# Kernel tuning notes

Hardware: AMD Instinct MI355X
Metric: run time of the kernel (lower is better)

The kernel has to match this reference:

```python
import jax, jax.numpy as jnp
import numpy as np

N_NODES = 100000
N_EDGES = 1600000
IN_DIM = 128
HID_DIM = 128


def setup_inputs() -> dict:
    key = jax.random.key(0)
    k_x, k_e, k_w1, k_w2 = jax.random.split(key, 4)
    x = jax.random.normal(k_x, (N_NODES, IN_DIM), dtype=jnp.float32)
    edge_index = jax.random.randint(k_e, (2, N_EDGES), 0, N_NODES, dtype=jnp.int64)
    # Glorot-style init like PyG GCNConv
    s1 = 1.0 / np.sqrt(IN_DIM)
    s2 = 1.0 / np.sqrt(HID_DIM)
    W1 = jax.random.uniform(k_w1, (IN_DIM, HID_DIM), jnp.float32, -s1, s1)
    b1 = jnp.zeros((HID_DIM,), jnp.float32)
    W2 = jax.random.uniform(k_w2, (HID_DIM, HID_DIM), jnp.float32, -s2, s2)
    b2 = jnp.zeros((HID_DIM,), jnp.float32)
    return {"x": x, "edge_index": edge_index, "W1": W1, "b1": b1, "W2": W2, "b2": b2}


def _gcn_norm(edge_index, num_nodes):
    # add self-loops, then symmetric normalization D^{-1/2} (A+I) D^{-1/2}
    loops = jnp.arange(num_nodes, dtype=edge_index.dtype)
    src = jnp.concatenate([edge_index[0], loops])
    dst = jnp.concatenate([edge_index[1], loops])
    deg = jax.ops.segment_sum(jnp.ones_like(dst, dtype=jnp.float32), dst,
                              num_segments=num_nodes)
    dinv = jnp.where(deg > 0, jax.lax.rsqrt(deg), 0.0)
    norm = dinv[src] * dinv[dst]  # [E + N]
    return src, dst, norm


def _gcn_conv(x, W, b, src, dst, norm, num_nodes):
    h = x @ W  # transform first (out_dim == in_dim here, order matches PyG)
    msg = h[src] * norm[:, None]  # gather + scale, [E+N, D]
    out = jax.ops.segment_sum(msg, dst, num_segments=num_nodes)
    return out + b


def reference(x, edge_index, W1, b1, W2, b2):
    n = x.shape[0]
    src, dst, norm = _gcn_norm(edge_index, n)
    h = _gcn_conv(x, W1, b1, src, dst, norm, n)
    h = jax.nn.relu(h)
    return _gcn_conv(h, W2, b2, src, dst, norm, n)
```

## Files before the change

### kernel.cpp

```cpp
#include <hip/hip_runtime.h>
#include <hip/hip_bf16.h>


#define NSEG 8
#define LHSZ 800
#define MAXB 4096

typedef unsigned int uint;
typedef unsigned short ushort;
typedef __attribute__((ext_vector_type(8))) short bf16x8;
typedef __attribute__((ext_vector_type(4))) float f32x4;

static __device__ __forceinline__ float bfl(uint u) { return __uint_as_float(u << 16); }
static __device__ __forceinline__ float bfh(uint u) { return __uint_as_float(u & 0xffff0000u); }
static __device__ __forceinline__ ushort f2bfu(float f) {
    __hip_bfloat16 b = __float2bfloat16(f);
    ushort u; __builtin_memcpy(&u, &b, 2); return u;
}
static __device__ __forceinline__ void splitT(float f, ushort& h, ushort& l) {
    uint u = __float_as_uint(f);
    h = (ushort)(u >> 16);
    float r = f - __uint_as_float(u & 0xffff0000u);
    l = (ushort)(__float_as_uint(r) >> 16);
}

__global__ __launch_bounds__(256) void wsplit_init(
    const float* __restrict__ W1, const float* __restrict__ W2,
    ushort* __restrict__ Ws1, ushort* __restrict__ Ws2,
    int* __restrict__ bcnt, int lenb)
{
    int tg = blockIdx.x * 256 + threadIdx.x;
    int w = tg >> 14;
    int e = tg & 16383;
    int k = e >> 7, n = e & 127;
    float f = (w ? W2 : W1)[e];
    ushort hi, lo; splitT(f, hi, lo);
    int I = (n * 128 + k) ^ ((n & 7) << 3);
    ushort* o = w ? Ws2 : Ws1;
    o[I] = hi; o[I + 16384] = lo;
    if (tg < lenb) bcnt[tg] = 0;
}

__global__ __launch_bounds__(1024) void scan_seg(
    const int* __restrict__ bcnt, int* __restrict__ ptr, int* __restrict__ cur,
    int len, int E)
{
    __shared__ int ws[16];
    int t = threadIdx.x, lane = t & 63, wv = t >> 6;
    int base = 0;
    for (int s0 = 0; s0 < len; s0 += 1024) {
        int i = s0 + t;
        int v = (i < len) ? bcnt[i] : 0;
        int x = v;
        #pragma unroll
        for (int d = 1; d < 64; d <<= 1) {
            int y = __shfl_up(x, d);
            if (lane >= d) x += y;
        }
        if (lane == 63) ws[wv] = x;
        __syncthreads();
        if (t < 16) {
            int sv = ws[t];
            #pragma unroll
            for (int d = 1; d < 16; d <<= 1) {
                int y = __shfl_up(sv, d);
                if (t >= d) sv += y;
            }
            ws[t] = sv;
        }
        __syncthreads();
        int wb = wv ? ws[wv - 1] : 0;
        int excl = base + wb + (x - v);
        if (i < len) { ptr[i] = excl; cur[i] = excl; }
        base += ws[15];
        __syncthreads();
    }
    if (t == 0) ptr[len] = E;
}

__global__ __launch_bounds__(256) void bucket_place(
    const int* __restrict__ src, const int* __restrict__ dst,
    int* __restrict__ cur, uint* __restrict__ ppack, int E, int nb, int epb)
{
    __shared__ int lhist[LHSZ];
    __shared__ int gb[LHSZ];
    int t = threadIdx.x;
    int seg = blockIdx.x & (NSEG - 1);
    int e0 = blockIdx.x * epb, e1 = min(E, e0 + epb);
    for (int i = t; i < nb; i += 256) lhist[i] = 0;
    __syncthreads();
    for (int e = e0 + t; e < e1; e += 256) atomicAdd(&lhist[dst[e] >> 7], 1);
    __syncthreads();
    for (int i = t; i < nb; i += 256) {
        int v = lhist[i];
        gb[i] = v ? atomicAdd(&cur[i * NSEG + seg], v) : 0;
        lhist[i] = 0;
    }
    __syncthreads();
    for (int e = e0 + t; e < e1; e += 256) {
        int d = dst[e];
        int b = d >> 7;
        int r = atomicAdd(&lhist[b], 1);
        ppack[gb[b] + r] = (uint)src[e] | ((uint)(d & 127) << 20);
    }
}

__global__ __launch_bounds__(256) void csr_finalize(
    const uint* __restrict__ ppack, const int* __restrict__ ptr,
    int* __restrict__ rowptr, int* __restrict__ csrsrc,
    float* __restrict__ dinv, int N, int E)
{
    __shared__ int ncnt[128], sbuf[128], ncur[128];
    __shared__ int srcbuf[MAXB];
    int t = threadIdx.x;
    int b = blockIdx.x;
    int node0 = b << 7;
    int nn = min(128, N - node0);
    int base = ptr[b * NSEG], end = ptr[(b + 1) * NSEG];
    int len = end - base;

    if (t < 128) ncnt[t] = 0;
    __syncthreads();
    for (int i = t; i < len; i += 256)
        atomicAdd(&ncnt[ppack[base + i] >> 20], 1);
    __syncthreads();
    if (t < 128) sbuf[t] = ncnt[t];
    __syncthreads();
    for (int d = 1; d < 128; d <<= 1) {
        int v = 0;
        if (t < 128 && t >= d) v = sbuf[t - d];
        __syncthreads();
        if (t < 128) sbuf[t] += v;
        __syncthreads();
    }
    if (t < 128) {
        int excl = sbuf[t] - ncnt[t];
        ncur[t] = excl;
        if (t < nn) {
            rowptr[node0 + t] = base + excl;
            dinv[node0 + t] = rsqrtf((float)(ncnt[t] + 1));
        }
    }
    __syncthreads();
    bool staged = (len <= MAXB);
    for (int i = t; i < len; i += 256) {
        uint p = ppack[base + i];
        int pos = atomicAdd(&ncur[p >> 20], 1);
        int sl = (int)(p & 0xFFFFFu);
        if (staged) srcbuf[pos] = sl;
        else        csrsrc[base + pos] = sl;
    }
    __syncthreads();
    if (staged)
        for (int i = t; i < len; i += 256) csrsrc[base + i] = srcbuf[i];
    if (b == 0 && t == 0) rowptr[N] = E;
}

template <int MODE>
static __device__ __forceinline__ void gemm_body(
    ushort* Wt, const void* __restrict__ Ap, const ushort* __restrict__ Wsp,
    ushort* __restrict__ out, int M, int blk)
{
    int t = threadIdx.x;
    {
        const uint4* s4 = (const uint4*)Wsp;
        uint4* d4 = (uint4*)Wt;
        #pragma unroll
        for (int j = 0; j < 16; ++j)
            d4[t + j * 256] = s4[t + j * 256];
    }
    __syncthreads();

    int wv = t >> 6, lane = t & 63;
    int g = lane >> 4;
    int lr = lane & 15;
    int rowbase = blk * 128 + wv * 32;
    int r0 = rowbase + lr, r1 = r0 + 16;
    int rc0 = min(r0, M - 1), rc1 = min(r1, M - 1);

    f32x4 acc[2][8];
    #pragma unroll
    for (int rt = 0; rt < 2; ++rt)
        #pragma unroll
        for (int ct = 0; ct < 8; ++ct)
            acc[rt][ct] = (f32x4)0.0f;

    #pragma unroll
    for (int ks = 0; ks < 4; ++ks) {
        int kof = ks * 32 + g * 8;
        bf16x8 ahi[2], alo[2];
        if (MODE == 0) {
            const float* A = (const float*)Ap;
            #pragma unroll
            for (int rt = 0; rt < 2; ++rt) {
                const float4* p = (const float4*)(A + (size_t)(rt ? rc1 : rc0) * 128 + kof);
                float4 u0 = p[0], u1 = p[1];
                float uu[8] = {u0.x, u0.y, u0.z, u0.w, u1.x, u1.y, u1.z, u1.w};
                bf16x8 ah, al;
                #pragma unroll
                for (int q = 0; q < 8; ++q) {
                    ushort hh, ll; splitT(uu[q], hh, ll);
                    ah[q] = (short)hh; al[q] = (short)ll;
                }
                ahi[rt] = ah; alo[rt] = al;
            }
        } else {
            const ushort* A = (const ushort*)Ap;
            ahi[0] = *(const bf16x8*)(A + (size_t)rc0 * 128 + kof);
            ahi[1] = *(const bf16x8*)(A + (size_t)rc1 * 128 + kof);
        }
        #pragma unroll
        for (int ct = 0; ct < 8; ++ct) {
            int n = ct * 16 + lr;
            int I = (n * 128 + kof) ^ ((n & 7) << 3);
            bf16x8 bhi = *(const bf16x8*)&Wt[I];
            bf16x8 blo = *(const bf16x8*)&Wt[I + 16384];
            #pragma unroll
            for (int rt = 0; rt < 2; ++rt) {
                acc[rt][ct] = __builtin_amdgcn_mfma_f32_16x16x32_bf16(ahi[rt], bhi, acc[rt][ct], 0, 0, 0);
                acc[rt][ct] = __builtin_amdgcn_mfma_f32_16x16x32_bf16(ahi[rt], blo, acc[rt][ct], 0, 0, 0);
                if (MODE == 0)
                    acc[rt][ct] = __builtin_amdgcn_mfma_f32_16x16x32_bf16(alo[rt], bhi, acc[rt][ct], 0, 0, 0);
            }
        }
    }

    #pragma unroll
    for (int rt = 0; rt < 2; ++rt) {
        #pragma unroll
        for (int r = 0; r < 4; ++r) {
            int row = rowbase + rt * 16 + g * 4 + r;
            if (row < M) {
                #pragma unroll
                for (int ct = 0; ct < 8; ++ct)
                    out[(size_t)row * 128 + ct * 16 + lr] = f2bfu(acc[rt][ct][r]);
            }
        }
    }
}

template <int MODE>
__global__ __launch_bounds__(256) void gemm_mfma(
    const void* __restrict__ Ap, const ushort* __restrict__ Wsp,
    ushort* __restrict__ out, int M)
{
    __shared__ ushort Wt[2 * 128 * 128];
    gemm_body<MODE>(Wt, Ap, Wsp, out, M, blockIdx.x);
}

__global__ __launch_bounds__(256) void gemm1_count(
    const float* __restrict__ x, const ushort* __restrict__ Wsp,
    ushort* __restrict__ h, int M, int gemmGrid,
    const int* __restrict__ dst, int* __restrict__ bcnt, int E, int nb, int epb)
{
    __shared__ ushort Wt[2 * 128 * 128];
    if ((int)blockIdx.x >= gemmGrid) {
        int* lhist = (int*)Wt;
        int b = blockIdx.x - gemmGrid;
        int t = threadIdx.x;
        int seg = b & (NSEG - 1);
        int e0 = b * epb, e1 = min(E, e0 + epb);
        for (int i = t; i < nb; i += 256) lhist[i] = 0;
        __syncthreads();
        for (int e = e0 + t; e < e1; e += 256) atomicAdd(&lhist[dst[e] >> 7], 1);
        __syncthreads();
        for (int i = t; i < nb; i += 256) {
            int v = lhist[i];
            if (v) atomicAdd(&bcnt[i * NSEG + seg], v);
        }
        return;
    }
    gemm_body<0>(Wt, x, Wsp, h, M, blockIdx.x);
}

#define FMA4(v, wgt) do { float wf_ = (wgt); \
    acc.x += bfl((v).x) * wf_; acc.y += bfh((v).x) * wf_; \
    acc.z += bfl((v).y) * wf_; acc.w += bfh((v).y) * wf_; } while (0)

template <bool RELU, bool OUTBF>
__global__ __launch_bounds__(1024) void agg_kernel(
    const ushort* __restrict__ h, const float* __restrict__ dinv,
    const int* __restrict__ rowptr, const int* __restrict__ csrsrc,
    const float* __restrict__ bias, void* __restrict__ outv, int n)
{
    __shared__ int2 epair[16][64];
    int t = threadIdx.x;
    int wv = t >> 6;
    int lane = t & 63;
    int half = lane >> 5, sub = lane & 31;
    int node = (blockIdx.x * 16 + wv) * 2 + half;
    bool active = node < n;
    int nodeC = active ? node : (n - 1);

    const uint2* h2 = (const uint2*)h;
    float di = dinv[nodeC];
    int beg = rowptr[nodeC];
    int m = rowptr[nodeC + 1] - beg;

    uint2 vs = h2[(size_t)nodeC * 32 + sub];
    float w0 = di * di;
    float4 acc;
    acc.x = bfl(vs.x) * w0; acc.y = bfh(vs.x) * w0;
    acc.z = bfl(vs.y) * w0; acc.w = bfh(vs.y) * w0;

    int mA = __shfl(m, 0), mB = __shfl(m, 32);
    int mmax = max(mA, mB);

    for (int eb = 0; eb < mmax; eb += 32) {
        int sl = 0; float dlw = 0.0f;
        if (active && (eb + sub) < m) {
            sl = csrsrc[beg + eb + sub];
            dlw = di * dinv[sl];
        }
        epair[wv][lane] = make_int2(sl, __float_as_int(dlw));
        int nq = mmax - eb; if (nq > 32) nq = 32;
        const int2* ep = &epair[wv][half * 32];
        for (int j = 0; j < nq; j += 8) {
            int2 p0 = ep[j + 0], p1 = ep[j + 1], p2 = ep[j + 2], p3 = ep[j + 3];
            int2 p4 = ep[j + 4], p5 = ep[j + 5], p6 = ep[j + 6], p7 = ep[j + 7];
            uint2 v0 = h2[(size_t)(uint)p0.x * 32 + sub];
            uint2 v1 = h2[(size_t)(uint)p1.x * 32 + sub];
            uint2 v2 = h2[(size_t)(uint)p2.x * 32 + sub];
            uint2 v3 = h2[(size_t)(uint)p3.x * 32 + sub];
            uint2 v4 = h2[(size_t)(uint)p4.x * 32 + sub];
            uint2 v5 = h2[(size_t)(uint)p5.x * 32 + sub];
            uint2 v6 = h2[(size_t)(uint)p6.x * 32 + sub];
            uint2 v7 = h2[(size_t)(uint)p7.x * 32 + sub];
            FMA4(v0, __int_as_float(p0.y));
            FMA4(v1, __int_as_float(p1.y));
            FMA4(v2, __int_as_float(p2.y));
            FMA4(v3, __int_as_float(p3.y));
            FMA4(v4, __int_as_float(p4.y));
            FMA4(v5, __int_as_float(p5.y));
            FMA4(v6, __int_as_float(p6.y));
            FMA4(v7, __int_as_float(p7.y));
        }
    }

    float4 bb = ((const float4*)bias)[sub];
    acc.x += bb.x; acc.y += bb.y; acc.z += bb.z; acc.w += bb.w;
    if (RELU) {
        acc.x = fmaxf(acc.x, 0.0f); acc.y = fmaxf(acc.y, 0.0f);
        acc.z = fmaxf(acc.z, 0.0f); acc.w = fmaxf(acc.w, 0.0f);
    }
    if (active) {
        if (OUTBF) {
            uint2 o;
            o.x = (uint)f2bfu(acc.x) | ((uint)f2bfu(acc.y) << 16);
            o.y = (uint)f2bfu(acc.z) | ((uint)f2bfu(acc.w) << 16);
            ((uint2*)outv)[(size_t)node * 32 + sub] = o;
        } else {
            ((float4*)outv)[(size_t)node * 32 + sub] = acc;
        }
    }
}

extern "C" void kernel_launch(void* const* d_in, const int* in_sizes, int n_in,
                              void* d_out, int out_size, void* d_ws, size_t ws_size,
                              hipStream_t stream)
{
    const float* x  = (const float*)d_in[0];
    const int*   ei = (const int*)d_in[1];
    const float* W1 = (const float*)d_in[2];
    const float* b1 = (const float*)d_in[3];
    const float* W2 = (const float*)d_in[4];
    const float* b2 = (const float*)d_in[5];

    const int N = in_sizes[0] / 128;
    const int E = in_sizes[1] / 2;
    const int* esrc = ei;
    const int* edst = ei + E;
    const int nb = (N + 127) >> 7;

    char* ws = (char*)d_ws;
    size_t off = 0;
    auto alloc = [&](size_t bytes) -> void* {
        void* p = ws + off;
        off += (bytes + 255) & ~(size_t)255;
        return p;
    };
    ushort* h      = (ushort*)alloc((size_t)N * 128 * sizeof(ushort));
    uint*   ppack  = (uint*)  alloc((size_t)E * sizeof(uint));
    int*    csrsrc = (int*)   alloc((size_t)E * sizeof(int));
    int*    rowptr = (int*)   alloc((size_t)(N + 1) * sizeof(int));
    float*  dinv   = (float*) alloc((size_t)N * sizeof(float));
    int*    bcnt   = (int*)   alloc((size_t)(NSEG * nb) * sizeof(int));
    int*    ptr    = (int*)   alloc((size_t)(NSEG * nb + 1) * sizeof(int));
    int*    cur    = (int*)   alloc((size_t)(NSEG * nb) * sizeof(int));
    ushort* Ws1    = (ushort*)alloc(2 * 128 * 128 * sizeof(ushort));
    ushort* Ws2    = (ushort*)alloc(2 * 128 * 128 * sizeof(ushort));

    const int gridA = 512;
    const int epb = (E + gridA - 1) / gridA;
    const int gemmGrid = (N + 127) / 128;

    wsplit_init<<<128, 256, 0, stream>>>(W1, W2, Ws1, Ws2, bcnt, NSEG * nb);
    gemm1_count<<<gemmGrid + gridA, 256, 0, stream>>>(x, Ws1, h, N, gemmGrid,
                                                      edst, bcnt, E, nb, epb);
    scan_seg<<<1, 1024, 0, stream>>>(bcnt, ptr, cur, NSEG * nb, E);
    bucket_place<<<gridA, 256, 0, stream>>>(esrc, edst, cur, ppack, E, nb, epb);
    csr_finalize<<<nb, 256, 0, stream>>>(ppack, ptr, rowptr, csrsrc, dinv, N, E);
    agg_kernel<true, true><<<(N + 31) / 32, 1024, 0, stream>>>(h, dinv, rowptr, csrsrc,
                                                               b1, d_out, N);
    gemm_mfma<1><<<gemmGrid, 256, 0, stream>>>(d_out, Ws2, h, N);
    agg_kernel<false, false><<<(N + 31) / 32, 1024, 0, stream>>>(h, dinv, rowptr, csrsrc,
                                                                 b2, d_out, N);
}
```

Measured before the change: 237.8 us.

## Precompute per-edge dinv in CSR, wave-per-node aggregation, global degree atomics

Computes node degrees with global atomics up front, derives dinv and per-bucket counts from them, and drops the 8-way segmented bucket counts. The CSR now stores (src, dinv[src]) pairs, so the aggregation kernel no longer does a dependent dinv lookup per edge. Aggregation is restructured to one 64-lane wave per node, with 16-edge unrolled gathers straight from global memory instead of LDS staging. The trade-offs are twice the edge-array bytes, contended global atomics on deg, and more idle lanes on low-degree nodes.

```diff
diff --git a/kernel.cpp b/kernel.cpp
--- a/kernel.cpp
+++ b/kernel.cpp
@@ -2,7 +2,6 @@
 #include <hip/hip_bf16.h>
 
 
-#define NSEG 8
 #define LHSZ 800
 #define MAXB 4096
 
@@ -24,21 +23,27 @@
     l = (ushort)(__float_as_uint(r) >> 16);
 }
 
-__global__ __launch_bounds__(256) void wsplit_init(
+__global__ __launch_bounds__(256) void wsplit_deg(
     const float* __restrict__ W1, const float* __restrict__ W2,
     ushort* __restrict__ Ws1, ushort* __restrict__ Ws2,
-    int* __restrict__ bcnt, int lenb)
-{
-    int tg = blockIdx.x * 256 + threadIdx.x;
-    int w = tg >> 14;
-    int e = tg & 16383;
-    int k = e >> 7, n = e & 127;
-    float f = (w ? W2 : W1)[e];
-    ushort hi, lo; splitT(f, hi, lo);
-    int I = (n * 128 + k) ^ ((n & 7) << 3);
-    ushort* o = w ? Ws2 : Ws1;
-    o[I] = hi; o[I + 16384] = lo;
-    if (tg < lenb) bcnt[tg] = 0;
+    const int* __restrict__ dst, int* __restrict__ deg, int E)
+{
+    int t = threadIdx.x;
+    if ((int)blockIdx.x < 128) {
+        int tg = blockIdx.x * 256 + t;
+        int w = tg >> 14;
+        int e = tg & 16383;
+        int k = e >> 7, n = e & 127;
+        float f = (w ? W2 : W1)[e];
+        ushort hi, lo; splitT(f, hi, lo);
+        int I = (n * 128 + k) ^ ((n & 7) << 3);
+        ushort* o = w ? Ws2 : Ws1;
+        o[I] = hi; o[I + 16384] = lo;
+        return;
+    }
+    int idx = (blockIdx.x - 128) * 256 + t;
+    for (int e = idx; e < E; e += 65536)
+        atomicAdd(&deg[dst[e]], 1);
 }
 
 __global__ __launch_bounds__(1024) void scan_seg(
@@ -85,7 +90,6 @@
     __shared__ int lhist[LHSZ];
     __shared__ int gb[LHSZ];
     int t = threadIdx.x;
-    int seg = blockIdx.x & (NSEG - 1);
     int e0 = blockIdx.x * epb, e1 = min(E, e0 + epb);
     for (int i = t; i < nb; i += 256) lhist[i] = 0;
     __syncthreads();
@@ -93,7 +97,7 @@
     __syncthreads();
     for (int i = t; i < nb; i += 256) {
         int v = lhist[i];
-        gb[i] = v ? atomicAdd(&cur[i * NSEG + seg], v) : 0;
+        gb[i] = v ? atomicAdd(&cur[i], v) : 0;
         lhist[i] = 0;
     }
     __syncthreads();
@@ -107,8 +111,8 @@
 
 __global__ __launch_bounds__(256) void csr_finalize(
     const uint* __restrict__ ppack, const int* __restrict__ ptr,
-    int* __restrict__ rowptr, int* __restrict__ csrsrc,
-    float* __restrict__ dinv, int N, int E)
+    const float* __restrict__ dinv,
+    int* __restrict__ rowptr, int2* __restrict__ epk, int N, int E)
 {
     __shared__ int ncnt[128], sbuf[128], ncur[128];
     __shared__ int srcbuf[MAXB];
@@ -116,7 +120,7 @@
     int b = blockIdx.x;
     int node0 = b << 7;
     int nn = min(128, N - node0);
-    int base = ptr[b * NSEG], end = ptr[(b + 1) * NSEG];
+    int base = ptr[b], end = ptr[b + 1];
     int len = end - base;
 
     if (t < 128) ncnt[t] = 0;
@@ -136,10 +140,7 @@
     if (t < 128) {
         int excl = sbuf[t] - ncnt[t];
         ncur[t] = excl;
-        if (t < nn) {
-            rowptr[node0 + t] = base + excl;
-            dinv[node0 + t] = rsqrtf((float)(ncnt[t] + 1));
-        }
+        if (t < nn) rowptr[node0 + t] = base + excl;
     }
     __syncthreads();
     bool staged = (len <= MAXB);
@@ -148,11 +149,14 @@
         int pos = atomicAdd(&ncur[p >> 20], 1);
         int sl = (int)(p & 0xFFFFFu);
         if (staged) srcbuf[pos] = sl;
-        else        csrsrc[base + pos] = sl;
+        else        epk[base + pos] = make_int2(sl, __float_as_int(dinv[sl]));
     }
     __syncthreads();
     if (staged)
-        for (int i = t; i < len; i += 256) csrsrc[base + i] = srcbuf[i];
+        for (int i = t; i < len; i += 256) {
+            int sl = srcbuf[i];
+            epk[base + i] = make_int2(sl, __float_as_int(dinv[sl]));
+        }
     if (b == 0 && t == 0) rowptr[N] = E;
 }
 
@@ -248,110 +252,90 @@
     gemm_body<MODE>(Wt, Ap, Wsp, out, M, blockIdx.x);
 }
 
-__global__ __launch_bounds__(256) void gemm1_count(
+__global__ __launch_bounds__(256) void gemm1_dinv(
     const float* __restrict__ x, const ushort* __restrict__ Wsp,
     ushort* __restrict__ h, int M, int gemmGrid,
-    const int* __restrict__ dst, int* __restrict__ bcnt, int E, int nb, int epb)
+    const int* __restrict__ deg, float* __restrict__ dinv,
+    int* __restrict__ bcnt, int N, int nb)
 {
     __shared__ ushort Wt[2 * 128 * 128];
     if ((int)blockIdx.x >= gemmGrid) {
-        int* lhist = (int*)Wt;
-        int b = blockIdx.x - gemmGrid;
+        __shared__ int wsum[4];
+        int bb = blockIdx.x - gemmGrid;
         int t = threadIdx.x;
-        int seg = b & (NSEG - 1);
-        int e0 = b * epb, e1 = min(E, e0 + epb);
-        for (int i = t; i < nb; i += 256) lhist[i] = 0;
-        __syncthreads();
-        for (int e = e0 + t; e < e1; e += 256) atomicAdd(&lhist[dst[e] >> 7], 1);
-        __syncthreads();
-        for (int i = t; i < nb; i += 256) {
-            int v = lhist[i];
-            if (v) atomicAdd(&bcnt[i * NSEG + seg], v);
+        int i = bb * 256 + t;
+        int d = (i < N) ? deg[i] : 0;
+        if (i < N) dinv[i] = rsqrtf((float)(d + 1));
+        int s = d;
+        #pragma unroll
+        for (int o = 1; o < 64; o <<= 1) s += __shfl_xor(s, o);
+        if ((t & 63) == 0) wsum[t >> 6] = s;
+        __syncthreads();
+        if (t == 0) {
+            int b0 = bb * 2;
+            if (b0 < nb)     bcnt[b0]     = wsum[0] + wsum[1];
+            if (b0 + 1 < nb) bcnt[b0 + 1] = wsum[2] + wsum[3];
         }
         return;
     }
     gemm_body<0>(Wt, x, Wsp, h, M, blockIdx.x);
 }
 
-#define FMA4(v, wgt) do { float wf_ = (wgt); \
-    acc.x += bfl((v).x) * wf_; acc.y += bfh((v).x) * wf_; \
-    acc.z += bfl((v).y) * wf_; acc.w += bfh((v).y) * wf_; } while (0)
-
 template <bool RELU, bool OUTBF>
-__global__ __launch_bounds__(1024) void agg_kernel(
+__global__ __launch_bounds__(256) void agg_kernel(
     const ushort* __restrict__ h, const float* __restrict__ dinv,
-    const int* __restrict__ rowptr, const int* __restrict__ csrsrc,
+    const int* __restrict__ rowptr, const int2* __restrict__ epk,
     const float* __restrict__ bias, void* __restrict__ outv, int n)
 {
-    __shared__ int2 epair[16][64];
-    int t = threadIdx.x;
-    int wv = t >> 6;
-    int lane = t & 63;
-    int half = lane >> 5, sub = lane & 31;
-    int node = (blockIdx.x * 16 + wv) * 2 + half;
-    bool active = node < n;
-    int nodeC = active ? node : (n - 1);
-
-    const uint2* h2 = (const uint2*)h;
-    float di = dinv[nodeC];
-    int beg = rowptr[nodeC];
-    int m = rowptr[nodeC + 1] - beg;
-
-    uint2 vs = h2[(size_t)nodeC * 32 + sub];
-    float w0 = di * di;
-    float4 acc;
-    acc.x = bfl(vs.x) * w0; acc.y = bfh(vs.x) * w0;
-    acc.z = bfl(vs.y) * w0; acc.w = bfh(vs.y) * w0;
-
-    int mA = __shfl(m, 0), mB = __shfl(m, 32);
-    int mmax = max(mA, mB);
-
-    for (int eb = 0; eb < mmax; eb += 32) {
-        int sl = 0; float dlw = 0.0f;
-        if (active && (eb + sub) < m) {
-            sl = csrsrc[beg + eb + sub];
-            dlw = di * dinv[sl];
-        }
-        epair[wv][lane] = make_int2(sl, __float_as_int(dlw));
-        int nq = mmax - eb; if (nq > 32) nq = 32;
-        const int2* ep = &epair[wv][half * 32];
-        for (int j = 0; j < nq; j += 8) {
-            int2 p0 = ep[j + 0], p1 = ep[j + 1], p2 = ep[j + 2], p3 = ep[j + 3];
-            int2 p4 = ep[j + 4], p5 = ep[j + 5], p6 = ep[j + 6], p7 = ep[j + 7];
-            uint2 v0 = h2[(size_t)(uint)p0.x * 32 + sub];
-            uint2 v1 = h2[(size_t)(uint)p1.x * 32 + sub];
-            uint2 v2 = h2[(size_t)(uint)p2.x * 32 + sub];
-            uint2 v3 = h2[(size_t)(uint)p3.x * 32 + sub];
-            uint2 v4 = h2[(size_t)(uint)p4.x * 32 + sub];
-            uint2 v5 = h2[(size_t)(uint)p5.x * 32 + sub];
-            uint2 v6 = h2[(size_t)(uint)p6.x * 32 + sub];
-            uint2 v7 = h2[(size_t)(uint)p7.x * 32 + sub];
-            FMA4(v0, __int_as_float(p0.y));
-            FMA4(v1, __int_as_float(p1.y));
-            FMA4(v2, __int_as_float(p2.y));
-            FMA4(v3, __int_as_float(p3.y));
-            FMA4(v4, __int_as_float(p4.y));
-            FMA4(v5, __int_as_float(p5.y));
-            FMA4(v6, __int_as_float(p6.y));
-            FMA4(v7, __int_as_float(p7.y));
-        }
-    }
-
-    float4 bb = ((const float4*)bias)[sub];
-    acc.x += bb.x; acc.y += bb.y; acc.z += bb.z; acc.w += bb.w;
-    if (RELU) {
-        acc.x = fmaxf(acc.x, 0.0f); acc.y = fmaxf(acc.y, 0.0f);
-        acc.z = fmaxf(acc.z, 0.0f); acc.w = fmaxf(acc.w, 0.0f);
-    }
-    if (active) {
-        if (OUTBF) {
-            uint2 o;
-            o.x = (uint)f2bfu(acc.x) | ((uint)f2bfu(acc.y) << 16);
-            o.y = (uint)f2bfu(acc.z) | ((uint)f2bfu(acc.w) << 16);
-            ((uint2*)outv)[(size_t)node * 32 + sub] = o;
-        } else {
-            ((float4*)outv)[(size_t)node * 32 + sub] = acc;
-        }
+    int wvU = __builtin_amdgcn_readfirstlane(threadIdx.x >> 6);
+    int lane = threadIdx.x & 63;
+    int node = blockIdx.x * 4 + wvU;
+    if (node >= n) return;
+
+    const uint* hr = (const uint*)h;
+    float di = dinv[node];
+    int beg = rowptr[node], end = rowptr[node + 1];
+
+    uint vs = hr[(size_t)node * 64 + lane];
+    float a0 = 0.0f, a1 = 0.0f, b0 = 0.0f, b1 = 0.0f;
+
+    int j = beg;
+    for (; j + 16 <= end; j += 16) {
+        int2 ee[16];
+        #pragma unroll
+        for (int k = 0; k < 16; ++k) ee[k] = epk[j + k];
+        uint vv[16];
+        #pragma unroll
+        for (int k = 0; k < 16; ++k)
+            vv[k] = hr[(size_t)(uint)ee[k].x * 64 + lane];
+        #pragma unroll
+        for (int k = 0; k < 16; k += 2) {
+            float w0 = __int_as_float(ee[k].y);
+            float w1 = __int_as_float(ee[k + 1].y);
+            a0 = fmaf(bfl(vv[k]), w0, a0);     a1 = fmaf(bfh(vv[k]), w0, a1);
+            b0 = fmaf(bfl(vv[k + 1]), w1, b0); b1 = fmaf(bfh(vv[k + 1]), w1, b1);
+        }
+    }
+    for (; j < end; ++j) {
+        int2 e = epk[j];
+        uint v = hr[(size_t)(uint)e.x * 64 + lane];
+        float w = __int_as_float(e.y);
+        a0 = fmaf(bfl(v), w, a0); a1 = fmaf(bfh(v), w, a1);
+    }
+    a0 += b0; a1 += b1;
+
+    float selfw = di * di;
+    a0 = a0 * di + bfl(vs) * selfw;
+    a1 = a1 * di + bfh(vs) * selfw;
+    float2 bb = ((const float2*)bias)[lane];
+    a0 += bb.x; a1 += bb.y;
+    if (RELU) { a0 = fmaxf(a0, 0.0f); a1 = fmaxf(a1, 0.0f); }
+
+    if (OUTBF) {
+        uint o = (uint)f2bfu(a0) | ((uint)f2bfu(a1) << 16);
+        ((uint*)outv)[(size_t)node * 64 + lane] = o;
+    } else {
+        ((float2*)outv)[(size_t)node * 64 + lane] = make_float2(a0, a1);
     }
 }
 
@@ -381,28 +365,31 @@
     };
     ushort* h      = (ushort*)alloc((size_t)N * 128 * sizeof(ushort));
     uint*   ppack  = (uint*)  alloc((size_t)E * sizeof(uint));
-    int*    csrsrc = (int*)   alloc((size_t)E * sizeof(int));
+    int2*   epk    = (int2*)  alloc((size_t)E * sizeof(int2));
     int*    rowptr = (int*)   alloc((size_t)(N + 1) * sizeof(int));
     float*  dinv   = (float*) alloc((size_t)N * sizeof(float));
-    int*    bcnt   = (int*)   alloc((size_t)(NSEG * nb) * sizeof(int));
-    int*    ptr    = (int*)   alloc((size_t)(NSEG * nb + 1) * sizeof(int));
-    int*    cur    = (int*)   alloc((size_t)(NSEG * nb) * sizeof(int));
+    int*    deg    = (int*)   alloc((size_t)N * sizeof(int));
+    int*    bcnt   = (int*)   alloc((size_t)nb * sizeof(int));
+    int*    ptr    = (int*)   alloc((size_t)(nb + 1) * sizeof(int));
+    int*    cur    = (int*)   alloc((size_t)nb * sizeof(int));
     ushort* Ws1    = (ushort*)alloc(2 * 128 * 128 * sizeof(ushort));
     ushort* Ws2    = (ushort*)alloc(2 * 128 * 128 * sizeof(ushort));
 
-    const int gridA = 512;
-    const int epb = (E + gridA - 1) / gridA;
+    const int gridP = 512;
+    const int epb = (E + gridP - 1) / gridP;
     const int gemmGrid = (N + 127) / 128;
-
-    wsplit_init<<<128, 256, 0, stream>>>(W1, W2, Ws1, Ws2, bcnt, NSEG * nb);
-    gemm1_count<<<gemmGrid + gridA, 256, 0, stream>>>(x, Ws1, h, N, gemmGrid,
-                                                      edst, bcnt, E, nb, epb);
-    scan_seg<<<1, 1024, 0, stream>>>(bcnt, ptr, cur, NSEG * nb, E);
-    bucket_place<<<gridA, 256, 0, stream>>>(esrc, edst, cur, ppack, E, nb, epb);
-    csr_finalize<<<nb, 256, 0, stream>>>(ppack, ptr, rowptr, csrsrc, dinv, N, E);
-    agg_kernel<true, true><<<(N + 31) / 32, 1024, 0, stream>>>(h, dinv, rowptr, csrsrc,
-                                                               b1, d_out, N);
+    const int dgrid = (N + 255) / 256;
+
+    hipMemsetAsync(deg, 0, (size_t)N * sizeof(int), stream);
+    wsplit_deg<<<128 + 256, 256, 0, stream>>>(W1, W2, Ws1, Ws2, edst, deg, E);
+    gemm1_dinv<<<gemmGrid + dgrid, 256, 0, stream>>>(x, Ws1, h, N, gemmGrid,
+                                                     deg, dinv, bcnt, N, nb);
+    scan_seg<<<1, 1024, 0, stream>>>(bcnt, ptr, cur, nb, E);
+    bucket_place<<<gridP, 256, 0, stream>>>(esrc, edst, cur, ppack, E, nb, epb);
+    csr_finalize<<<nb, 256, 0, stream>>>(ppack, ptr, dinv, rowptr, epk, N, E);
+    agg_kernel<true, true><<<(N + 3) / 4, 256, 0, stream>>>(h, dinv, rowptr, epk,
+                                                            b1, d_out, N);
     gemm_mfma<1><<<gemmGrid, 256, 0, stream>>>(d_out, Ws2, h, N);
-    agg_kernel<false, false><<<(N + 31) / 32, 1024, 0, stream>>>(h, dinv, rowptr, csrsrc,
-                                                                 b2, d_out, N);
-}
+    agg_kernel<false, false><<<(N + 3) / 4, 256, 0, stream>>>(h, dinv, rowptr, epk,
+                                                              b2, d_out, N);
+}
```

Measured after the change: 305.2 us. 1.28x slower.
